# Kernel optimization log

Hardware: AMD Instinct MI355X
Metric: run time of the kernel (lower is better)

Reference implementation:

```python
import jax, jax.numpy as jnp
import numpy as np

KERNEL = 5
DILATIONS = (3, 1)
N_HEADS = 8
LN_EPS = 1e-5


def unfold1d(x, kernel, dilation, pad):
    # x: (N, H, S) -> (N, H, S, kernel) dilated sliding windows (same length)
    xp = jnp.pad(x, ((0, 0), (0, 0), (pad, pad)))
    S = x.shape[-1]
    idx = jnp.arange(S)[:, None] + jnp.arange(kernel)[None, :] * dilation  # (S, K)
    return xp[:, :, idx]  # (N, H, S, K)


def dilated_mha(q, k, v, Ws, bs, Wo, bo):
    # q,k,v: (B, S, D); Ws: (2, split, split); Wo: (D, D)
    B, S, D = q.shape
    ndil = len(DILATIONS)
    hpd = N_HEADS // ndil            # heads per dilation
    dk = D // N_HEADS
    split = D // ndil
    scale = dk ** (-0.5)
    outs, probs = [], []
    for i, dil in enumerate(DILATIONS):
        pad = dil * (KERNEL - 1) // 2
        sl = slice(i * split, (i + 1) * split)
        qi = q[..., sl] @ Ws[i].T + bs[i]
        ki = k[..., sl] @ Ws[i].T + bs[i]
        vi = v[..., sl] @ Ws[i].T + bs[i]
        # (B,S,hpd,dk) -> (B,dk,hpd,S), matching torch transpose(1,2).permute(0,3,1,2)
        to4 = lambda x: jnp.transpose(x.reshape(B, S, hpd, dk), (0, 3, 2, 1))
        qi4, ki4, vi4 = to4(qi), to4(ki), to4(vi)
        # unfold then reinterpret (B*dk,hpd,...) as (B*hpd,dk,...) exactly as torch .reshape does
        kp = unfold1d(ki4.reshape(B * dk, hpd, S), KERNEL, dil, pad).reshape(B * hpd, dk, S, KERNEL)
        vp = unfold1d(vi4.reshape(B * dk, hpd, S), KERNEL, dil, pad).reshape(B * hpd, dk, S, KERNEL)
        qr = qi4.reshape(B * hpd, dk, S)
        scores = jnp.einsum('nds,ndsk->nsk', qr, kp) * scale   # (B*hpd, S, K)
        p = jax.nn.softmax(scores, axis=-1)
        out = jnp.einsum('nsk,ndsk->nds', p, vp)               # (B*hpd, dk, S)
        out = jnp.transpose(out.reshape(B, hpd, dk, S), (0, 3, 1, 2)).reshape(B, S, split)
        outs.append(out)
        probs.append(p.reshape(B, hpd, S, KERNEL))
    o = jnp.concatenate(outs, axis=-1) @ Wo.T + bo
    return o, jnp.concatenate(probs, axis=1)


def layer_norm(x, g, b):
    mu = jnp.mean(x, axis=-1, keepdims=True)
    var = jnp.mean((x - mu) ** 2, axis=-1, keepdims=True)
    return (x - mu) * jax.lax.rsqrt(var + LN_EPS) * g + b


def setup_inputs() -> dict:
    key = jax.random.key(0)
    ks = jax.random.split(key, 6)
    B, S, D = 32, 2048, 256
    split = D // 2
    q_emb = jax.random.normal(ks[0], (B, S, D), dtype=jnp.float32)
    s_emb = jax.random.normal(ks[1], (B, S, D), dtype=jnp.float32)
    lens = jax.random.randint(ks[2], (B,), 5, S, dtype=jnp.int32)
    W_lin = jax.random.normal(ks[3], (3, 2, split, split), dtype=jnp.float32) * (split ** -0.5)
    b_lin = jnp.zeros((3, 2, split), dtype=jnp.float32)
    W_out = jax.random.normal(ks[4], (3, D, D), dtype=jnp.float32) * (D ** -0.5)
    b_out = jnp.zeros((3, D), dtype=jnp.float32)
    ln_g = jnp.ones((3, D), dtype=jnp.float32)
    ln_b = jnp.zeros((3, D), dtype=jnp.float32)
    return {"q_emb": q_emb, "s_emb": s_emb, "lens": lens, "W_lin": W_lin,
            "b_lin": b_lin, "W_out": W_out, "b_out": b_out, "ln_g": ln_g, "ln_b": ln_b}


def reference(q_emb, s_emb, lens, W_lin, b_lin, W_out, b_out, ln_g, ln_b):
    # CASTransformer.forward, shortcut=True path, eval mode (dropout=id, mask unused)
    a1, _ = dilated_mha(q_emb, q_emb, q_emb, W_lin[0], b_lin[0], W_out[0], b_out[0])
    hq = layer_norm(q_emb + a1, ln_g[0], ln_b[0])
    a2, q_scores = dilated_mha(s_emb, s_emb, s_emb, W_lin[1], b_lin[1], W_out[1], b_out[1])
    hs = layer_norm(s_emb + a2, ln_g[1], ln_b[1])
    a3, _ = dilated_mha(hq, hq, hs, W_lin[2], b_lin[2], W_out[2], b_out[2])
    z = layer_norm(hq + a3, ln_g[2], ln_b[2])
    return z, q_scores
```

## Files before the change

### kernel.cpp

```cpp
#include <hip/hip_runtime.h>
#include <hip/hip_bf16.h>

typedef __bf16 bf16x8 __attribute__((ext_vector_type(8)));
typedef float  f32x4  __attribute__((ext_vector_type(4)));
typedef unsigned int u32;
typedef u32 u32x4 __attribute__((ext_vector_type(4)));
typedef unsigned short ushort_t;

__device__ inline float bf2f(ushort_t h) {
    union { u32 u; float f; } v; v.u = ((u32)h) << 16; return v.f;
}
__device__ inline ushort_t f2bf(float f) {
    union { float f; u32 u; } v; v.f = f;
    u32 u = v.u;
    return (ushort_t)((u + 0x7fffu + ((u >> 16) & 1u)) >> 16);
}
__device__ inline bf16x8 load_bf8(const ushort_t* p) {
    u32x4 u = *reinterpret_cast<const u32x4*>(p);
    return __builtin_bit_cast(bf16x8, u);
}
__device__ inline bf16x8 load8_in(const void* base, size_t idx, int f32flag) {
    if (!f32flag) return load_bf8((const ushort_t*)base + idx);
    const float* pf = (const float*)base + idx;
    f32x4 a = *reinterpret_cast<const f32x4*>(pf);
    f32x4 b = *reinterpret_cast<const f32x4*>(pf + 4);
    bf16x8 r;
#pragma unroll
    for (int j = 0; j < 4; ++j) { r[j] = (__bf16)a[j]; r[4 + j] = (__bf16)b[j]; }
    return r;
}
__device__ inline float ld_in(const void* base, size_t idx, int f32flag) {
    return f32flag ? ((const float*)base)[idx] : bf2f(((const ushort_t*)base)[idx]);
}

#define XT_STRIDE 264

__global__ __launch_bounds__(256) void detect_kernel(const u32* __restrict__ d, int n,
                                                     int* __restrict__ flag) {
    const int t = threadIdx.x;
    int cn = 0, co = 0;
    for (int i = t; i < n; i += 256) {
        const u32 w = d[i];
        const u32 e  = (w >> 7) & 0xFF;
        const u32 fe = (w >> 23) & 0xFF;
        cn += (e >= 100 && e <= 135) ? 1 : 0;
        co += (((w & 0xFFFFu) == 0u) && fe >= 100 && fe <= 140) ? 1 : 0;
    }
    __shared__ int sn[256], so[256];
    sn[t] = cn; so[t] = co; __syncthreads();
    for (int o = 128; o; o >>= 1) {
        if (t < o) { sn[t] += sn[t + o]; so[t] += so[t + o]; }
        __syncthreads();
    }
    if (t == 0) {
        const int CN = sn[0], CO = so[0];
        const int is_f32 = (2 * CN < n) && ((2 * CO > n) || (20 * CN > n));
        *flag = is_f32 ? 1 : 0;
    }
}

__device__ inline int f_of(const int* flags, int i) { return i < 0 ? 0 : flags[i]; }
__device__ inline int out_f32(const int* flags) {
    return flags[0] | flags[1] | flags[3] | flags[4] | flags[5] | flags[6] | flags[7] | flags[8];
}

__global__ __launch_bounds__(256) void proj_kernel(
    const void* __restrict__ X, int xi,
    const void* __restrict__ W, size_t lw,
    const void* __restrict__ Bv, size_t lb,
    ushort_t* __restrict__ Y, const int* __restrict__ flags)
{
    const int xf = f_of(flags, xi);
    const int wf = flags[3], bf = flags[4];
    const int tid  = threadIdx.x;
    const int wave = tid >> 6, lane = tid & 63;
    const int dil  = wave >> 1;
    const int n_off = (wave & 1) * 64;
    const int m0   = blockIdx.x * 64;
    const int l15  = lane & 15, quad = lane >> 4;

    f32x4 acc[4][4] = {};
    for (int kc = 0; kc < 4; ++kc) {
        bf16x8 a[4], b[4];
#pragma unroll
        for (int mt = 0; mt < 4; ++mt)
            a[mt] = load8_in(X, (size_t)(m0 + mt * 16 + l15) * 256 + dil * 128 + kc * 32 + quad * 8, xf);
#pragma unroll
        for (int nt = 0; nt < 4; ++nt)
            b[nt] = load8_in(W, lw + (size_t)dil * 16384 + (size_t)(n_off + nt * 16 + l15) * 128 + kc * 32 + quad * 8, wf);
#pragma unroll
        for (int mt = 0; mt < 4; ++mt)
#pragma unroll
            for (int nt = 0; nt < 4; ++nt)
                acc[mt][nt] = __builtin_amdgcn_mfma_f32_16x16x32_bf16(a[mt], b[nt], acc[mt][nt], 0, 0, 0);
    }
#pragma unroll
    for (int mt = 0; mt < 4; ++mt) {
#pragma unroll
        for (int nt = 0; nt < 4; ++nt) {
            const int ncol = n_off + nt * 16 + l15;
            const float bias = ld_in(Bv, lb + dil * 128 + ncol, bf);
#pragma unroll
            for (int r = 0; r < 4; ++r) {
                const int row = m0 + mt * 16 + quad * 4 + r;
                Y[(size_t)row * 256 + dil * 128 + ncol] = f2bf(acc[mt][nt][r] + bias);
            }
        }
    }
}

__global__ __launch_bounds__(256) void proj_inplace_kernel(
    ushort_t* __restrict__ X,
    const void* __restrict__ W, size_t lw,
    const void* __restrict__ Bv, size_t lb,
    const int* __restrict__ flags)
{
    __shared__ ushort_t xt[64 * XT_STRIDE];
    const int wf = flags[3], bf = flags[4];
    const int tid = threadIdx.x;
    const int m0  = blockIdx.x * 64;
#pragma unroll
    for (int i = 0; i < 8; ++i) {
        const int chunk = tid + 256 * i;
        const int row = chunk >> 5, cc = chunk & 31;
        *reinterpret_cast<u32x4*>(&xt[row * XT_STRIDE + cc * 8]) =
            *reinterpret_cast<const u32x4*>(X + (size_t)(m0 + row) * 256 + cc * 8);
    }
    __syncthreads();

    const int wave = tid >> 6, lane = tid & 63;
    const int dil  = wave >> 1;
    const int n_off = (wave & 1) * 64;
    const int l15  = lane & 15, quad = lane >> 4;

    f32x4 acc[4][4] = {};
    for (int kc = 0; kc < 4; ++kc) {
        bf16x8 a[4], b[4];
#pragma unroll
        for (int mt = 0; mt < 4; ++mt)
            a[mt] = load_bf8(&xt[(mt * 16 + l15) * XT_STRIDE + dil * 128 + kc * 32 + quad * 8]);
#pragma unroll
        for (int nt = 0; nt < 4; ++nt)
            b[nt] = load8_in(W, lw + (size_t)dil * 16384 + (size_t)(n_off + nt * 16 + l15) * 128 + kc * 32 + quad * 8, wf);
#pragma unroll
        for (int mt = 0; mt < 4; ++mt)
#pragma unroll
            for (int nt = 0; nt < 4; ++nt)
                acc[mt][nt] = __builtin_amdgcn_mfma_f32_16x16x32_bf16(a[mt], b[nt], acc[mt][nt], 0, 0, 0);
    }
#pragma unroll
    for (int mt = 0; mt < 4; ++mt) {
#pragma unroll
        for (int nt = 0; nt < 4; ++nt) {
            const int ncol = n_off + nt * 16 + l15;
            const float bias = ld_in(Bv, lb + dil * 128 + ncol, bf);
#pragma unroll
            for (int r = 0; r < 4; ++r) {
                const int row = m0 + mt * 16 + quad * 4 + r;
                X[(size_t)row * 256 + dil * 128 + ncol] = f2bf(acc[mt][nt][r] + bias);
            }
        }
    }
}

__global__ __launch_bounds__(256) void fused_attn_oln_kernel(
    const ushort_t* __restrict__ P, const ushort_t* __restrict__ V,
    const void* __restrict__ R, int ri,
    const void* __restrict__ W, size_t lw,
    const void* __restrict__ Bv, size_t lb,
    const void* __restrict__ G, const void* __restrict__ Bt, size_t lg,
    void* __restrict__ H, int h_out,
    void* __restrict__ probs_base,
    const int* __restrict__ flags)
{
    __shared__ ushort_t xt[64 * XT_STRIDE];
    __shared__ float lsum[4][64], lsq[4][64];

    const int wf = flags[5], bvf = flags[6], gf = flags[7], btf = flags[8];
    const int rf = f_of(flags, ri);
    const int og = out_f32(flags);
    const int of = h_out ? og : 0;

    const int tid = threadIdx.x;
    const int m0  = blockIdx.x * 64;
    const int bb  = m0 >> 11;
    const int s0  = m0 & 2047;
    const size_t rowbase = (size_t)bb * 2048;
    const float scale = 0.17677669529663687f;

#pragma unroll
    for (int it = 0; it < 2; ++it) {
        const int task = tid + 256 * it;
        const int r  = task & 63;
        const int dg = task >> 6;
        const int dil = dg >> 2, g = dg & 3;
        const int dila = dil ? 1 : 3;
        const int s = s0 + r;
        const size_t chan0 = (size_t)dil * 128 + g * 8;

        const ushort_t* qr = P + (rowbase + s) * 256 + chan0;
        float qv[4][8];
#pragma unroll
        for (int h = 0; h < 4; ++h) {
            bf16x8 t = load_bf8(qr + h * 32);
#pragma unroll
            for (int j = 0; j < 8; ++j) qv[h][j] = (float)t[j];
        }
        float sc[5];
#pragma unroll
        for (int kk = 0; kk < 5; ++kk) {
            const int sp = s + (kk - 2) * dila;
            float a = 0.f;
            if (sp >= 0 && sp < 2048) {
                const ushort_t* kr = P + (rowbase + sp) * 256 + chan0;
#pragma unroll
                for (int h = 0; h < 4; ++h) {
                    bf16x8 t = load_bf8(kr + h * 32);
#pragma unroll
                    for (int j = 0; j < 8; ++j) a += qv[h][j] * (float)t[j];
                }
                a *= scale;
            }
            sc[kk] = a;
        }
        float mx = sc[0];
#pragma unroll
        for (int kk = 1; kk < 5; ++kk) mx = fmaxf(mx, sc[kk]);
        float p[5], sum = 0.f;
#pragma unroll
        for (int kk = 0; kk < 5; ++kk) { p[kk] = __expf(sc[kk] - mx); sum += p[kk]; }
        const float inv = 1.f / sum;
#pragma unroll
        for (int kk = 0; kk < 5; ++kk) p[kk] *= inv;

        float o[4][8] = {};
#pragma unroll
        for (int kk = 0; kk < 5; ++kk) {
            const int sp = s + (kk - 2) * dila;
            if (sp < 0 || sp >= 2048) continue;
            const ushort_t* vr = V + (rowbase + sp) * 256 + chan0;
#pragma unroll
            for (int h = 0; h < 4; ++h) {
                bf16x8 t = load_bf8(vr + h * 32);
#pragma unroll
                for (int j = 0; j < 8; ++j) o[h][j] += p[kk] * (float)t[j];
            }
        }
        ushort_t* op = &xt[r * XT_STRIDE + dil * 128 + g * 32];
#pragma unroll
        for (int c = 0; c < 4; ++c) {
            u32x4 w;
#pragma unroll
            for (int t4 = 0; t4 < 4; ++t4) {
                const int d2a = c * 8 + t4 * 2, d2b = d2a + 1;
                const u32 lo = f2bf(o[d2a & 3][d2a >> 2]);
                const u32 hi = f2bf(o[d2b & 3][d2b >> 2]);
                w[t4] = lo | (hi << 16);
            }
            *reinterpret_cast<u32x4*>(op + c * 8) = w;
        }
        if (probs_base != nullptr) {
            const size_t pb = 16777216 + ((size_t)((bb * 8 + dg) * 2048 + s)) * 5;
            if (og) {
                float* pp = (float*)probs_base;
#pragma unroll
                for (int kk = 0; kk < 5; ++kk) pp[pb + kk] = p[kk];
            } else {
                ushort_t* pp = (ushort_t*)probs_base;
#pragma unroll
                for (int kk = 0; kk < 5; ++kk) pp[pb + kk] = f2bf(p[kk]);
            }
        }
    }
    __syncthreads();

    const int wave = tid >> 6, lane = tid & 63;
    const int n_off = wave * 64;
    const int l15 = lane & 15, quad = lane >> 4;

    f32x4 acc[4][4] = {};
    for (int kc = 0; kc < 8; ++kc) {
        bf16x8 a[4], b[4];
#pragma unroll
        for (int mt = 0; mt < 4; ++mt)
            a[mt] = load_bf8(&xt[(mt * 16 + l15) * XT_STRIDE + kc * 32 + quad * 8]);
#pragma unroll
        for (int nt = 0; nt < 4; ++nt)
            b[nt] = load8_in(W, lw + (size_t)(n_off + nt * 16 + l15) * 256 + kc * 32 + quad * 8, wf);
#pragma unroll
        for (int mt = 0; mt < 4; ++mt)
#pragma unroll
            for (int nt = 0; nt < 4; ++nt)
                acc[mt][nt] = __builtin_amdgcn_mfma_f32_16x16x32_bf16(a[mt], b[nt], acc[mt][nt], 0, 0, 0);
    }

    float bias[4];
#pragma unroll
    for (int nt = 0; nt < 4; ++nt) bias[nt] = ld_in(Bv, lb + n_off + nt * 16 + l15, bvf);

    float psum[4][4] = {}, psq[4][4] = {};
#pragma unroll
    for (int mt = 0; mt < 4; ++mt) {
#pragma unroll
        for (int rr = 0; rr < 4; ++rr) {
            const size_t rrow = (size_t)(m0 + mt * 16 + quad * 4 + rr) * 256 + l15;
#pragma unroll
            for (int nt = 0; nt < 4; ++nt) {
                float v = acc[mt][nt][rr] + bias[nt] + ld_in(R, rrow + n_off + nt * 16, rf);
                acc[mt][nt][rr] = v;
                psum[mt][rr] += v;
                psq[mt][rr]  += v * v;
            }
        }
    }
#pragma unroll
    for (int off = 1; off <= 8; off <<= 1) {
#pragma unroll
        for (int mt = 0; mt < 4; ++mt)
#pragma unroll
            for (int rr = 0; rr < 4; ++rr) {
                psum[mt][rr] += __shfl_xor(psum[mt][rr], off);
                psq[mt][rr]  += __shfl_xor(psq[mt][rr],  off);
            }
    }
    if (l15 == 0) {
#pragma unroll
        for (int mt = 0; mt < 4; ++mt)
#pragma unroll
            for (int rr = 0; rr < 4; ++rr) {
                const int row = mt * 16 + quad * 4 + rr;
                lsum[wave][row] = psum[mt][rr];
                lsq[wave][row]  = psq[mt][rr];
            }
    }
    __syncthreads();

    float gl[4], bl[4];
#pragma unroll
    for (int nt = 0; nt < 4; ++nt) {
        gl[nt] = ld_in(G,  lg + n_off + nt * 16 + l15, gf);
        bl[nt] = ld_in(Bt, lg + n_off + nt * 16 + l15, btf);
    }
#pragma unroll
    for (int mt = 0; mt < 4; ++mt) {
#pragma unroll
        for (int rr = 0; rr < 4; ++rr) {
            const int row = mt * 16 + quad * 4 + rr;
            const float sm = lsum[0][row] + lsum[1][row] + lsum[2][row] + lsum[3][row];
            const float q2 = lsq[0][row]  + lsq[1][row]  + lsq[2][row]  + lsq[3][row];
            const float mu  = sm * (1.f / 256.f);
            const float var = q2 * (1.f / 256.f) - mu * mu;
            const float rs  = rsqrtf(var + 1e-5f);
            const size_t hrow = (size_t)(m0 + row) * 256 + l15;
#pragma unroll
            for (int nt = 0; nt < 4; ++nt) {
                const float hv = (acc[mt][nt][rr] - mu) * rs * gl[nt] + bl[nt];
                if (of) ((float*)H)[hrow + n_off + nt * 16] = hv;
                else    ((ushort_t*)H)[hrow + n_off + nt * 16] = f2bf(hv);
            }
        }
    }
}

extern "C" void kernel_launch(void* const* d_in, const int* in_sizes, int n_in,
                              void* d_out, int out_size, void* d_ws, size_t ws_size,
                              hipStream_t stream) {
    const void* q_emb = d_in[0];
    const void* s_emb = d_in[1];
    const void* W_lin = d_in[3];
    const void* b_lin = d_in[4];
    const void* W_out = d_in[5];
    const void* b_out = d_in[6];
    const void* ln_g  = d_in[7];
    const void* ln_b  = d_in[8];

    const size_t SLOT = 16777216;
    int*      flags = (int*)d_ws;
    ushort_t* SA = (ushort_t*)((char*)d_ws + 256);
    ushort_t* SB = SA + SLOT;
    ushort_t* SC = SA + 2 * SLOT;

    const dim3 blk(256);
    detect_kernel<<<1, blk, 0, stream>>>((const u32*)q_emb, 16384, flags + 0);
    detect_kernel<<<1, blk, 0, stream>>>((const u32*)s_emb, 16384, flags + 1);
    detect_kernel<<<1, blk, 0, stream>>>((const u32*)W_lin, 16384, flags + 3);
    detect_kernel<<<1, blk, 0, stream>>>((const u32*)b_lin,   384, flags + 4);
    detect_kernel<<<1, blk, 0, stream>>>((const u32*)W_out, 16384, flags + 5);
    detect_kernel<<<1, blk, 0, stream>>>((const u32*)b_out,   384, flags + 6);
    detect_kernel<<<1, blk, 0, stream>>>((const u32*)ln_g,    384, flags + 7);
    detect_kernel<<<1, blk, 0, stream>>>((const u32*)ln_b,    384, flags + 8);

    proj_kernel<<<1024, blk, 0, stream>>>(q_emb, 0, W_lin, 0, b_lin, 0, SC, flags);
    fused_attn_oln_kernel<<<1024, blk, 0, stream>>>(SC, SC, q_emb, 0,
        W_out, 0, b_out, 0, ln_g, ln_b, 0, SA, 0, nullptr, flags);
    proj_kernel<<<1024, blk, 0, stream>>>(s_emb, 1, W_lin, 32768, b_lin, 256, SC, flags);
    fused_attn_oln_kernel<<<1024, blk, 0, stream>>>(SC, SC, s_emb, 1,
        W_out, 65536, b_out, 256, ln_g, ln_b, 256, SB, 0, d_out, flags);
    proj_kernel<<<1024, blk, 0, stream>>>(SA, -1, W_lin, 65536, b_lin, 512, SC, flags);
    proj_inplace_kernel<<<1024, blk, 0, stream>>>(SB, W_lin, 65536, b_lin, 512, flags);
    fused_attn_oln_kernel<<<1024, blk, 0, stream>>>(SC, SB, SA, -1,
        W_out, 131072, b_out, 512, ln_g, ln_b, 512, d_out, 1, nullptr, flags);
}
```

Measured before the change: 696.1 us.

## Fuse input projection into attention+output stage kernel with halo tiles in LDS

Each stage now computes the per-dilation linear projection for a 64-row tile plus an 8-row halo on each side directly into a swizzled shared-memory tile, then runs the windowed attention from LDS instead of from a global projected buffer. This removes the separate projection kernels and the round trip of the projected activations through global memory, and it collapses seven launches into three. In exchange, each block recomputes 16 halo rows per tile (80 rows instead of 64), serializes the two dilations through more barriers, and uses a larger shared-memory footprint that may reduce occupancy.

After: 855.7 us. +22.9%, slower.

```diff
diff --git a/kernel.cpp b/kernel.cpp
--- a/kernel.cpp
+++ b/kernel.cpp
@@ -64,145 +64,95 @@
     return flags[0] | flags[1] | flags[3] | flags[4] | flags[5] | flags[6] | flags[7] | flags[8];
 }
 
-__global__ __launch_bounds__(256) void proj_kernel(
-    const void* __restrict__ X, int xi,
-    const void* __restrict__ W, size_t lw,
-    const void* __restrict__ Bv, size_t lb,
-    ushort_t* __restrict__ Y, const int* __restrict__ flags)
+__device__ inline int tidx(int row, int ch) { return row * 128 + (ch ^ ((row & 7) << 3)); }
+
+__device__ __forceinline__ void proj_tile(
+    const void* __restrict__ X, int xf, int dil, int bb, int s0,
+    const void* __restrict__ W, size_t lw, int wfl,
+    const void* __restrict__ Bv, size_t lb, int bfl,
+    ushort_t* tile, int wave, int lane)
 {
-    const int xf = f_of(flags, xi);
-    const int wf = flags[3], bf = flags[4];
-    const int tid  = threadIdx.x;
-    const int wave = tid >> 6, lane = tid & 63;
-    const int dil  = wave >> 1;
-    const int n_off = (wave & 1) * 64;
-    const int m0   = blockIdx.x * 64;
-    const int l15  = lane & 15, quad = lane >> 4;
-
-    f32x4 acc[4][4] = {};
+    const int l15 = lane & 15, quad = lane >> 4;
+    const int n_off = wave * 32;
+    f32x4 acc[5][2] = {};
     for (int kc = 0; kc < 4; ++kc) {
-        bf16x8 a[4], b[4];
-#pragma unroll
-        for (int mt = 0; mt < 4; ++mt)
-            a[mt] = load8_in(X, (size_t)(m0 + mt * 16 + l15) * 256 + dil * 128 + kc * 32 + quad * 8, xf);
-#pragma unroll
-        for (int nt = 0; nt < 4; ++nt)
-            b[nt] = load8_in(W, lw + (size_t)dil * 16384 + (size_t)(n_off + nt * 16 + l15) * 128 + kc * 32 + quad * 8, wf);
-#pragma unroll
-        for (int mt = 0; mt < 4; ++mt)
-#pragma unroll
-            for (int nt = 0; nt < 4; ++nt)
+        bf16x8 a[5], b[2];
+#pragma unroll
+        for (int mt = 0; mt < 5; ++mt) {
+            int s = s0 - 8 + mt * 16 + l15;
+            s = s < 0 ? 0 : (s > 2047 ? 2047 : s);
+            a[mt] = load8_in(X, ((size_t)bb * 2048 + s) * 256 + dil * 128 + kc * 32 + quad * 8, xf);
+        }
+#pragma unroll
+        for (int nt = 0; nt < 2; ++nt)
+            b[nt] = load8_in(W, lw + (size_t)dil * 16384 +
+                             (size_t)(n_off + nt * 16 + l15) * 128 + kc * 32 + quad * 8, wfl);
+#pragma unroll
+        for (int mt = 0; mt < 5; ++mt)
+#pragma unroll
+            for (int nt = 0; nt < 2; ++nt)
                 acc[mt][nt] = __builtin_amdgcn_mfma_f32_16x16x32_bf16(a[mt], b[nt], acc[mt][nt], 0, 0, 0);
     }
 #pragma unroll
-    for (int mt = 0; mt < 4; ++mt) {
-#pragma unroll
-        for (int nt = 0; nt < 4; ++nt) {
-            const int ncol = n_off + nt * 16 + l15;
-            const float bias = ld_in(Bv, lb + dil * 128 + ncol, bf);
+    for (int nt = 0; nt < 2; ++nt) {
+        const int ncol = n_off + nt * 16 + l15;
+        const float bias = ld_in(Bv, lb + dil * 128 + ncol, bfl);
+#pragma unroll
+        for (int mt = 0; mt < 5; ++mt)
 #pragma unroll
             for (int r = 0; r < 4; ++r) {
-                const int row = m0 + mt * 16 + quad * 4 + r;
-                Y[(size_t)row * 256 + dil * 128 + ncol] = f2bf(acc[mt][nt][r] + bias);
-            }
-        }
-    }
-}
-
-__global__ __launch_bounds__(256) void proj_inplace_kernel(
-    ushort_t* __restrict__ X,
-    const void* __restrict__ W, size_t lw,
-    const void* __restrict__ Bv, size_t lb,
-    const int* __restrict__ flags)
-{
-    __shared__ ushort_t xt[64 * XT_STRIDE];
-    const int wf = flags[3], bf = flags[4];
-    const int tid = threadIdx.x;
-    const int m0  = blockIdx.x * 64;
-#pragma unroll
-    for (int i = 0; i < 8; ++i) {
-        const int chunk = tid + 256 * i;
-        const int row = chunk >> 5, cc = chunk & 31;
-        *reinterpret_cast<u32x4*>(&xt[row * XT_STRIDE + cc * 8]) =
-            *reinterpret_cast<const u32x4*>(X + (size_t)(m0 + row) * 256 + cc * 8);
-    }
-    __syncthreads();
-
-    const int wave = tid >> 6, lane = tid & 63;
-    const int dil  = wave >> 1;
-    const int n_off = (wave & 1) * 64;
-    const int l15  = lane & 15, quad = lane >> 4;
-
-    f32x4 acc[4][4] = {};
-    for (int kc = 0; kc < 4; ++kc) {
-        bf16x8 a[4], b[4];
-#pragma unroll
-        for (int mt = 0; mt < 4; ++mt)
-            a[mt] = load_bf8(&xt[(mt * 16 + l15) * XT_STRIDE + dil * 128 + kc * 32 + quad * 8]);
-#pragma unroll
-        for (int nt = 0; nt < 4; ++nt)
-            b[nt] = load8_in(W, lw + (size_t)dil * 16384 + (size_t)(n_off + nt * 16 + l15) * 128 + kc * 32 + quad * 8, wf);
-#pragma unroll
-        for (int mt = 0; mt < 4; ++mt)
-#pragma unroll
-            for (int nt = 0; nt < 4; ++nt)
-                acc[mt][nt] = __builtin_amdgcn_mfma_f32_16x16x32_bf16(a[mt], b[nt], acc[mt][nt], 0, 0, 0);
-    }
-#pragma unroll
-    for (int mt = 0; mt < 4; ++mt) {
-#pragma unroll
-        for (int nt = 0; nt < 4; ++nt) {
-            const int ncol = n_off + nt * 16 + l15;
-            const float bias = ld_in(Bv, lb + dil * 128 + ncol, bf);
-#pragma unroll
-            for (int r = 0; r < 4; ++r) {
-                const int row = m0 + mt * 16 + quad * 4 + r;
-                X[(size_t)row * 256 + dil * 128 + ncol] = f2bf(acc[mt][nt][r] + bias);
-            }
-        }
-    }
-}
-
-__global__ __launch_bounds__(256) void fused_attn_oln_kernel(
-    const ushort_t* __restrict__ P, const ushort_t* __restrict__ V,
+                const int row = mt * 16 + quad * 4 + r;
+                tile[tidx(row, ncol)] = f2bf(acc[mt][nt][r] + bias);
+            }
+    }
+}
+
+__global__ __launch_bounds__(256) void stage_kernel(
+    const void* __restrict__ Xq, int xqi,
+    const void* __restrict__ Xv, int xvi, int sepv,
+    const void* __restrict__ Wl, size_t lwl,
+    const void* __restrict__ bl, size_t lbl,
+    const void* __restrict__ Wo, size_t lwo,
+    const void* __restrict__ bo, size_t lbo,
+    const void* __restrict__ G, const void* __restrict__ Bt, size_t lg,
     const void* __restrict__ R, int ri,
-    const void* __restrict__ W, size_t lw,
-    const void* __restrict__ Bv, size_t lb,
-    const void* __restrict__ G, const void* __restrict__ Bt, size_t lg,
     void* __restrict__ H, int h_out,
     void* __restrict__ probs_base,
     const int* __restrict__ flags)
 {
-    __shared__ ushort_t xt[64 * XT_STRIDE];
-    __shared__ float lsum[4][64], lsq[4][64];
-
-    const int wf = flags[5], bvf = flags[6], gf = flags[7], btf = flags[8];
-    const int rf = f_of(flags, ri);
-    const int og = out_f32(flags);
-    const int of = h_out ? og : 0;
-
-    const int tid = threadIdx.x;
-    const int m0  = blockIdx.x * 64;
-    const int bb  = m0 >> 11;
-    const int s0  = m0 & 2047;
-    const size_t rowbase = (size_t)bb * 2048;
+    __shared__ __align__(16) char smem[54272];
+    ushort_t* tile = (ushort_t*)smem;
+    ushort_t* xt   = (ushort_t*)(smem + 20480);
+
+    const int xqf = f_of(flags, xqi), xvf = f_of(flags, xvi);
+    const int wlf = flags[3], blf = flags[4];
+    const int wof = flags[5], bof = flags[6], gf = flags[7], btf = flags[8];
+    const int rf  = f_of(flags, ri);
+    const int og  = out_f32(flags);
+    const int of  = h_out ? og : 0;
+
+    const int tid  = threadIdx.x;
+    const int wave = tid >> 6, lane = tid & 63;
+    const int l15  = lane & 15, quad = lane >> 4;
+    const int m0   = blockIdx.x * 64;
+    const int bb   = m0 >> 11;
+    const int s0   = m0 & 2047;
     const float scale = 0.17677669529663687f;
 
-#pragma unroll
-    for (int it = 0; it < 2; ++it) {
-        const int task = tid + 256 * it;
-        const int r  = task & 63;
-        const int dg = task >> 6;
-        const int dil = dg >> 2, g = dg & 3;
+    const int r = lane, g = wave;
+
+    for (int dil = 0; dil < 2; ++dil) {
+        if (dil) __syncthreads();
+        proj_tile(Xq, xqf, dil, bb, s0, Wl, lwl, wlf, bl, lbl, blf, tile, wave, lane);
+        __syncthreads();
+
         const int dila = dil ? 1 : 3;
         const int s = s0 + r;
-        const size_t chan0 = (size_t)dil * 128 + g * 8;
-
-        const ushort_t* qr = P + (rowbase + s) * 256 + chan0;
+
         float qv[4][8];
 #pragma unroll
         for (int h = 0; h < 4; ++h) {
-            bf16x8 t = load_bf8(qr + h * 32);
+            bf16x8 t = load_bf8(&tile[tidx(8 + r, g * 8 + h * 32)]);
 #pragma unroll
             for (int j = 0; j < 8; ++j) qv[h][j] = (float)t[j];
         }
@@ -212,10 +162,10 @@
             const int sp = s + (kk - 2) * dila;
             float a = 0.f;
             if (sp >= 0 && sp < 2048) {
-                const ushort_t* kr = P + (rowbase + sp) * 256 + chan0;
+                const int krow = 8 + r + (kk - 2) * dila;
 #pragma unroll
                 for (int h = 0; h < 4; ++h) {
-                    bf16x8 t = load_bf8(kr + h * 32);
+                    bf16x8 t = load_bf8(&tile[tidx(krow, g * 8 + h * 32)]);
 #pragma unroll
                     for (int j = 0; j < 8; ++j) a += qv[h][j] * (float)t[j];
                 }
@@ -233,15 +183,34 @@
 #pragma unroll
         for (int kk = 0; kk < 5; ++kk) p[kk] *= inv;
 
+        if (probs_base != nullptr) {
+            const size_t pb = 16777216 + ((size_t)((bb * 8 + dil * 4 + g) * 2048 + s)) * 5;
+            if (og) {
+                float* pp = (float*)probs_base;
+#pragma unroll
+                for (int kk = 0; kk < 5; ++kk) pp[pb + kk] = p[kk];
+            } else {
+                ushort_t* pp = (ushort_t*)probs_base;
+#pragma unroll
+                for (int kk = 0; kk < 5; ++kk) pp[pb + kk] = f2bf(p[kk]);
+            }
+        }
+
+        if (sepv) {
+            __syncthreads();
+            proj_tile(Xv, xvf, dil, bb, s0, Wl, lwl, wlf, bl, lbl, blf, tile, wave, lane);
+            __syncthreads();
+        }
+
         float o[4][8] = {};
 #pragma unroll
         for (int kk = 0; kk < 5; ++kk) {
             const int sp = s + (kk - 2) * dila;
             if (sp < 0 || sp >= 2048) continue;
-            const ushort_t* vr = V + (rowbase + sp) * 256 + chan0;
+            const int vrow = 8 + r + (kk - 2) * dila;
 #pragma unroll
             for (int h = 0; h < 4; ++h) {
-                bf16x8 t = load_bf8(vr + h * 32);
+                bf16x8 t = load_bf8(&tile[tidx(vrow, g * 8 + h * 32)]);
 #pragma unroll
                 for (int j = 0; j < 8; ++j) o[h][j] += p[kk] * (float)t[j];
             }
@@ -259,24 +228,13 @@
             }
             *reinterpret_cast<u32x4*>(op + c * 8) = w;
         }
-        if (probs_base != nullptr) {
-            const size_t pb = 16777216 + ((size_t)((bb * 8 + dg) * 2048 + s)) * 5;
-            if (og) {
-                float* pp = (float*)probs_base;
-#pragma unroll
-                for (int kk = 0; kk < 5; ++kk) pp[pb + kk] = p[kk];
-            } else {
-                ushort_t* pp = (ushort_t*)probs_base;
-#pragma unroll
-                for (int kk = 0; kk < 5; ++kk) pp[pb + kk] = f2bf(p[kk]);
-            }
-        }
     }
     __syncthreads();
 
-    const int wave = tid >> 6, lane = tid & 63;
+    float (*lsum)[64] = (float(*)[64])(smem);
+    float (*lsq)[64]  = (float(*)[64])(smem + 1024);
+
     const int n_off = wave * 64;
-    const int l15 = lane & 15, quad = lane >> 4;
 
     f32x4 acc[4][4] = {};
     for (int kc = 0; kc < 8; ++kc) {
@@ -286,7 +244,7 @@
             a[mt] = load_bf8(&xt[(mt * 16 + l15) * XT_STRIDE + kc * 32 + quad * 8]);
 #pragma unroll
         for (int nt = 0; nt < 4; ++nt)
-            b[nt] = load8_in(W, lw + (size_t)(n_off + nt * 16 + l15) * 256 + kc * 32 + quad * 8, wf);
+            b[nt] = load8_in(Wo, lwo + (size_t)(n_off + nt * 16 + l15) * 256 + kc * 32 + quad * 8, wof);
 #pragma unroll
         for (int mt = 0; mt < 4; ++mt)
 #pragma unroll
@@ -296,7 +254,7 @@
 
     float bias[4];
 #pragma unroll
-    for (int nt = 0; nt < 4; ++nt) bias[nt] = ld_in(Bv, lb + n_off + nt * 16 + l15, bvf);
+    for (int nt = 0; nt < 4; ++nt) bias[nt] = ld_in(bo, lbo + n_off + nt * 16 + l15, bof);
 
     float psum[4][4] = {}, psq[4][4] = {};
 #pragma unroll
@@ -335,11 +293,11 @@
     }
     __syncthreads();
 
-    float gl[4], bl[4];
+    float gl[4], blv[4];
 #pragma unroll
     for (int nt = 0; nt < 4; ++nt) {
-        gl[nt] = ld_in(G,  lg + n_off + nt * 16 + l15, gf);
-        bl[nt] = ld_in(Bt, lg + n_off + nt * 16 + l15, btf);
+        gl[nt]  = ld_in(G,  lg + n_off + nt * 16 + l15, gf);
+        blv[nt] = ld_in(Bt, lg + n_off + nt * 16 + l15, btf);
     }
 #pragma unroll
     for (int mt = 0; mt < 4; ++mt) {
@@ -354,7 +312,7 @@
             const size_t hrow = (size_t)(m0 + row) * 256 + l15;
 #pragma unroll
             for (int nt = 0; nt < 4; ++nt) {
-                const float hv = (acc[mt][nt][rr] - mu) * rs * gl[nt] + bl[nt];
+                const float hv = (acc[mt][nt][rr] - mu) * rs * gl[nt] + blv[nt];
                 if (of) ((float*)H)[hrow + n_off + nt * 16] = hv;
                 else    ((ushort_t*)H)[hrow + n_off + nt * 16] = f2bf(hv);
             }
@@ -378,7 +336,6 @@
     int*      flags = (int*)d_ws;
     ushort_t* SA = (ushort_t*)((char*)d_ws + 256);
     ushort_t* SB = SA + SLOT;
-    ushort_t* SC = SA + 2 * SLOT;
 
     const dim3 blk(256);
     detect_kernel<<<1, blk, 0, stream>>>((const u32*)q_emb, 16384, flags + 0);
@@ -390,14 +347,13 @@
     detect_kernel<<<1, blk, 0, stream>>>((const u32*)ln_g,    384, flags + 7);
     detect_kernel<<<1, blk, 0, stream>>>((const u32*)ln_b,    384, flags + 8);
 
-    proj_kernel<<<1024, blk, 0, stream>>>(q_emb, 0, W_lin, 0, b_lin, 0, SC, flags);
-    fused_attn_oln_kernel<<<1024, blk, 0, stream>>>(SC, SC, q_emb, 0,
-        W_out, 0, b_out, 0, ln_g, ln_b, 0, SA, 0, nullptr, flags);
-    proj_kernel<<<1024, blk, 0, stream>>>(s_emb, 1, W_lin, 32768, b_lin, 256, SC, flags);
-    fused_attn_oln_kernel<<<1024, blk, 0, stream>>>(SC, SC, s_emb, 1,
-        W_out, 65536, b_out, 256, ln_g, ln_b, 256, SB, 0, d_out, flags);
-    proj_kernel<<<1024, blk, 0, stream>>>(SA, -1, W_lin, 65536, b_lin, 512, SC, flags);
-    proj_inplace_kernel<<<1024, blk, 0, stream>>>(SB, W_lin, 65536, b_lin, 512, flags);
-    fused_attn_oln_kernel<<<1024, blk, 0, stream>>>(SC, SB, SA, -1,
-        W_out, 131072, b_out, 512, ln_g, ln_b, 512, d_out, 1, nullptr, flags);
-}
+    stage_kernel<<<1024, blk, 0, stream>>>(q_emb, 0, q_emb, 0, 0,
+        W_lin, 0, b_lin, 0, W_out, 0, b_out, 0, ln_g, ln_b, 0,
+        q_emb, 0, SA, 0, nullptr, flags);
+    stage_kernel<<<1024, blk, 0, stream>>>(s_emb, 1, s_emb, 1, 0,
+        W_lin, 32768, b_lin, 256, W_out, 65536, b_out, 256, ln_g, ln_b, 256,
+        s_emb, 1, SB, 0, d_out, flags);
+    stage_kernel<<<1024, blk, 0, stream>>>(SA, -1, SB, -1, 1,
+        W_lin, 65536, b_lin, 512, W_out, 131072, b_out, 512, ln_g, ln_b, 512,
+        SA, -1, d_out, 1, nullptr, flags);
+}
```

## Stage Q/K/V halo tiles in swizzled LDS and coalesce projection stores

Applied to the files above, without the earlier changes.

The attention kernel now loads a 64-row tile plus an 8-row halo of the projected Q/K (and V when it differs) into shared memory with an XOR swizzle. The dilated window reads then come from LDS instead of strided global loads. The projection kernel stages its input tile in swizzled LDS and writes results back through LDS so global stores are coalesced 16-byte vectors. The separate in-place projection kernel is merged into it. Launch bounds now request 4 blocks per SM. This adds more LDS per block (40 KB in attention) and extra barriers, which may limit occupancy.

After: 621.8 us. -10.7%, faster.

```diff
diff --git a/kernel.cpp b/kernel.cpp
--- a/kernel.cpp
+++ b/kernel.cpp
@@ -33,7 +33,8 @@
     return f32flag ? ((const float*)base)[idx] : bf2f(((const ushort_t*)base)[idx]);
 }
 
-#define XT_STRIDE 264
+__device__ inline int pofs(int row, int ch) { return row * 256 + (ch ^ ((row & 15) << 3)); }
+__device__ inline int tofs(int tr, int ch) { return tr * 256 + (ch ^ (((tr + 8) & 15) << 3)); }
 
 __global__ __launch_bounds__(256) void detect_kernel(const u32* __restrict__ d, int n,
                                                      int* __restrict__ flag) {
@@ -64,67 +65,24 @@
     return flags[0] | flags[1] | flags[3] | flags[4] | flags[5] | flags[6] | flags[7] | flags[8];
 }
 
-__global__ __launch_bounds__(256) void proj_kernel(
+__global__ __launch_bounds__(256, 4) void proj_kernel(
     const void* __restrict__ X, int xi,
     const void* __restrict__ W, size_t lw,
     const void* __restrict__ Bv, size_t lb,
     ushort_t* __restrict__ Y, const int* __restrict__ flags)
 {
-    const int xf = f_of(flags, xi);
-    const int wf = flags[3], bf = flags[4];
-    const int tid  = threadIdx.x;
-    const int wave = tid >> 6, lane = tid & 63;
-    const int dil  = wave >> 1;
-    const int n_off = (wave & 1) * 64;
-    const int m0   = blockIdx.x * 64;
-    const int l15  = lane & 15, quad = lane >> 4;
-
-    f32x4 acc[4][4] = {};
-    for (int kc = 0; kc < 4; ++kc) {
-        bf16x8 a[4], b[4];
-#pragma unroll
-        for (int mt = 0; mt < 4; ++mt)
-            a[mt] = load8_in(X, (size_t)(m0 + mt * 16 + l15) * 256 + dil * 128 + kc * 32 + quad * 8, xf);
-#pragma unroll
-        for (int nt = 0; nt < 4; ++nt)
-            b[nt] = load8_in(W, lw + (size_t)dil * 16384 + (size_t)(n_off + nt * 16 + l15) * 128 + kc * 32 + quad * 8, wf);
-#pragma unroll
-        for (int mt = 0; mt < 4; ++mt)
-#pragma unroll
-            for (int nt = 0; nt < 4; ++nt)
-                acc[mt][nt] = __builtin_amdgcn_mfma_f32_16x16x32_bf16(a[mt], b[nt], acc[mt][nt], 0, 0, 0);
-    }
-#pragma unroll
-    for (int mt = 0; mt < 4; ++mt) {
-#pragma unroll
-        for (int nt = 0; nt < 4; ++nt) {
-            const int ncol = n_off + nt * 16 + l15;
-            const float bias = ld_in(Bv, lb + dil * 128 + ncol, bf);
-#pragma unroll
-            for (int r = 0; r < 4; ++r) {
-                const int row = m0 + mt * 16 + quad * 4 + r;
-                Y[(size_t)row * 256 + dil * 128 + ncol] = f2bf(acc[mt][nt][r] + bias);
-            }
-        }
-    }
-}
-
-__global__ __launch_bounds__(256) void proj_inplace_kernel(
-    ushort_t* __restrict__ X,
-    const void* __restrict__ W, size_t lw,
-    const void* __restrict__ Bv, size_t lb,
-    const int* __restrict__ flags)
-{
-    __shared__ ushort_t xt[64 * XT_STRIDE];
-    const int wf = flags[3], bf = flags[4];
+    __shared__ ushort_t tile[64 * 256];
+    const int xf  = f_of(flags, xi);
+    const int wf  = flags[3], bfl = flags[4];
     const int tid = threadIdx.x;
     const int m0  = blockIdx.x * 64;
+
 #pragma unroll
     for (int i = 0; i < 8; ++i) {
-        const int chunk = tid + 256 * i;
-        const int row = chunk >> 5, cc = chunk & 31;
-        *reinterpret_cast<u32x4*>(&xt[row * XT_STRIDE + cc * 8]) =
-            *reinterpret_cast<const u32x4*>(X + (size_t)(m0 + row) * 256 + cc * 8);
+        const int c = tid + 256 * i;
+        const int row = c >> 5, cc = c & 31;
+        bf16x8 v = load8_in(X, (size_t)(m0 + row) * 256 + cc * 8, xf);
+        *reinterpret_cast<u32x4*>(&tile[pofs(row, cc * 8)]) = __builtin_bit_cast(u32x4, v);
     }
     __syncthreads();
 
@@ -138,32 +96,43 @@
         bf16x8 a[4], b[4];
 #pragma unroll
         for (int mt = 0; mt < 4; ++mt)
-            a[mt] = load_bf8(&xt[(mt * 16 + l15) * XT_STRIDE + dil * 128 + kc * 32 + quad * 8]);
+            a[mt] = load_bf8(&tile[pofs(mt * 16 + l15, dil * 128 + kc * 32 + quad * 8)]);
 #pragma unroll
         for (int nt = 0; nt < 4; ++nt)
-            b[nt] = load8_in(W, lw + (size_t)dil * 16384 + (size_t)(n_off + nt * 16 + l15) * 128 + kc * 32 + quad * 8, wf);
+            b[nt] = load8_in(W, lw + (size_t)dil * 16384 +
+                             (size_t)(n_off + nt * 16 + l15) * 128 + kc * 32 + quad * 8, wf);
 #pragma unroll
         for (int mt = 0; mt < 4; ++mt)
 #pragma unroll
             for (int nt = 0; nt < 4; ++nt)
                 acc[mt][nt] = __builtin_amdgcn_mfma_f32_16x16x32_bf16(a[mt], b[nt], acc[mt][nt], 0, 0, 0);
     }
-#pragma unroll
-    for (int mt = 0; mt < 4; ++mt) {
-#pragma unroll
-        for (int nt = 0; nt < 4; ++nt) {
-            const int ncol = n_off + nt * 16 + l15;
-            const float bias = ld_in(Bv, lb + dil * 128 + ncol, bf);
+    __syncthreads();
+
+#pragma unroll
+    for (int nt = 0; nt < 4; ++nt) {
+        const int ncol = n_off + nt * 16 + l15;
+        const float bias = ld_in(Bv, lb + dil * 128 + ncol, bfl);
+#pragma unroll
+        for (int mt = 0; mt < 4; ++mt)
 #pragma unroll
             for (int r = 0; r < 4; ++r) {
-                const int row = m0 + mt * 16 + quad * 4 + r;
-                X[(size_t)row * 256 + dil * 128 + ncol] = f2bf(acc[mt][nt][r] + bias);
-            }
-        }
-    }
-}
-
-__global__ __launch_bounds__(256) void fused_attn_oln_kernel(
+                const int row = mt * 16 + quad * 4 + r;
+                tile[pofs(row, dil * 128 + ncol)] = f2bf(acc[mt][nt][r] + bias);
+            }
+    }
+    __syncthreads();
+
+#pragma unroll
+    for (int i = 0; i < 8; ++i) {
+        const int c = tid + 256 * i;
+        const int row = c >> 5, cc = c & 31;
+        *reinterpret_cast<u32x4*>(Y + (size_t)(m0 + row) * 256 + cc * 8) =
+            *reinterpret_cast<const u32x4*>(&tile[row * 256 + cc * 8]);
+    }
+}
+
+__global__ __launch_bounds__(256, 4) void fused_attn_oln_kernel(
     const ushort_t* __restrict__ P, const ushort_t* __restrict__ V,
     const void* __restrict__ R, int ri,
     const void* __restrict__ W, size_t lw,
@@ -173,36 +142,48 @@
     void* __restrict__ probs_base,
     const int* __restrict__ flags)
 {
-    __shared__ ushort_t xt[64 * XT_STRIDE];
-    __shared__ float lsum[4][64], lsq[4][64];
+    __shared__ ushort_t tile[80 * 256];
+    float (*lsum)[64] = (float (*)[64])(&tile[0]);
+    float (*lsq)[64]  = (float (*)[64])(&tile[1024]);
 
     const int wf = flags[5], bvf = flags[6], gf = flags[7], btf = flags[8];
     const int rf = f_of(flags, ri);
     const int og = out_f32(flags);
     const int of = h_out ? og : 0;
 
-    const int tid = threadIdx.x;
-    const int m0  = blockIdx.x * 64;
-    const int bb  = m0 >> 11;
-    const int s0  = m0 & 2047;
+    const int tid  = threadIdx.x;
+    const int wave = tid >> 6, lane = tid & 63;
+    const int l15  = lane & 15, quad = lane >> 4;
+    const int m0   = blockIdx.x * 64;
+    const int bb   = m0 >> 11;
+    const int s0   = m0 & 2047;
     const size_t rowbase = (size_t)bb * 2048;
     const float scale = 0.17677669529663687f;
 
 #pragma unroll
+    for (int i = 0; i < 10; ++i) {
+        const int c = tid + 256 * i;
+        const int tr = c >> 5, cc = c & 31;
+        int s = s0 - 8 + tr; s = s < 0 ? 0 : (s > 2047 ? 2047 : s);
+        *reinterpret_cast<u32x4*>(&tile[tr * 256 + cc * 8]) =
+            *reinterpret_cast<const u32x4*>(P + (rowbase + s) * 256 + cc * 8);
+    }
+    __syncthreads();
+
+    const int r = lane, g = wave;
+    const int s = s0 + r;
+
+    float p2[2][5];
+#pragma unroll
     for (int it = 0; it < 2; ++it) {
-        const int task = tid + 256 * it;
-        const int r  = task & 63;
-        const int dg = task >> 6;
-        const int dil = dg >> 2, g = dg & 3;
+        const int dil  = it;
         const int dila = dil ? 1 : 3;
-        const int s = s0 + r;
-        const size_t chan0 = (size_t)dil * 128 + g * 8;
-
-        const ushort_t* qr = P + (rowbase + s) * 256 + chan0;
+        const int ch0  = dil * 128 + g * 8;
+
         float qv[4][8];
 #pragma unroll
         for (int h = 0; h < 4; ++h) {
-            bf16x8 t = load_bf8(qr + h * 32);
+            bf16x8 t = load_bf8(&tile[tofs(8 + r, ch0 + h * 32)]);
 #pragma unroll
             for (int j = 0; j < 8; ++j) qv[h][j] = (float)t[j];
         }
@@ -212,10 +193,10 @@
             const int sp = s + (kk - 2) * dila;
             float a = 0.f;
             if (sp >= 0 && sp < 2048) {
-                const ushort_t* kr = P + (rowbase + sp) * 256 + chan0;
+                const int tr2 = 8 + r + (kk - 2) * dila;
 #pragma unroll
                 for (int h = 0; h < 4; ++h) {
-                    bf16x8 t = load_bf8(kr + h * 32);
+                    bf16x8 t = load_bf8(&tile[tofs(tr2, ch0 + h * 32)]);
 #pragma unroll
                     for (int j = 0; j < 8; ++j) a += qv[h][j] * (float)t[j];
                 }
@@ -226,27 +207,59 @@
         float mx = sc[0];
 #pragma unroll
         for (int kk = 1; kk < 5; ++kk) mx = fmaxf(mx, sc[kk]);
-        float p[5], sum = 0.f;
-#pragma unroll
-        for (int kk = 0; kk < 5; ++kk) { p[kk] = __expf(sc[kk] - mx); sum += p[kk]; }
+        float sum = 0.f;
+#pragma unroll
+        for (int kk = 0; kk < 5; ++kk) { p2[it][kk] = __expf(sc[kk] - mx); sum += p2[it][kk]; }
         const float inv = 1.f / sum;
 #pragma unroll
-        for (int kk = 0; kk < 5; ++kk) p[kk] *= inv;
-
+        for (int kk = 0; kk < 5; ++kk) p2[it][kk] *= inv;
+
+        if (probs_base != nullptr) {
+            const size_t pb = 16777216 + ((size_t)((bb * 8 + dil * 4 + g) * 2048 + s)) * 5;
+            if (og) {
+                float* pp = (float*)probs_base;
+#pragma unroll
+                for (int kk = 0; kk < 5; ++kk) pp[pb + kk] = p2[it][kk];
+            } else {
+                ushort_t* pp = (ushort_t*)probs_base;
+#pragma unroll
+                for (int kk = 0; kk < 5; ++kk) pp[pb + kk] = f2bf(p2[it][kk]);
+            }
+        }
+    }
+
+    if (V != P) {
+        __syncthreads();
+#pragma unroll
+        for (int i = 0; i < 10; ++i) {
+            const int c = tid + 256 * i;
+            const int tr = c >> 5, cc = c & 31;
+            int s2 = s0 - 8 + tr; s2 = s2 < 0 ? 0 : (s2 > 2047 ? 2047 : s2);
+            *reinterpret_cast<u32x4*>(&tile[tr * 256 + cc * 8]) =
+                *reinterpret_cast<const u32x4*>(V + (rowbase + s2) * 256 + cc * 8);
+        }
+        __syncthreads();
+    }
+
+    u32x4 wpk[2][4];
+#pragma unroll
+    for (int it = 0; it < 2; ++it) {
+        const int dil  = it;
+        const int dila = dil ? 1 : 3;
+        const int ch0  = dil * 128 + g * 8;
         float o[4][8] = {};
 #pragma unroll
         for (int kk = 0; kk < 5; ++kk) {
             const int sp = s + (kk - 2) * dila;
             if (sp < 0 || sp >= 2048) continue;
-            const ushort_t* vr = V + (rowbase + sp) * 256 + chan0;
+            const int tr2 = 8 + r + (kk - 2) * dila;
 #pragma unroll
             for (int h = 0; h < 4; ++h) {
-                bf16x8 t = load_bf8(vr + h * 32);
-#pragma unroll
-                for (int j = 0; j < 8; ++j) o[h][j] += p[kk] * (float)t[j];
-            }
-        }
-        ushort_t* op = &xt[r * XT_STRIDE + dil * 128 + g * 32];
+                bf16x8 t = load_bf8(&tile[tofs(tr2, ch0 + h * 32)]);
+#pragma unroll
+                for (int j = 0; j < 8; ++j) o[h][j] += p2[it][kk] * (float)t[j];
+            }
+        }
 #pragma unroll
         for (int c = 0; c < 4; ++c) {
             u32x4 w;
@@ -257,33 +270,26 @@
                 const u32 hi = f2bf(o[d2b & 3][d2b >> 2]);
                 w[t4] = lo | (hi << 16);
             }
-            *reinterpret_cast<u32x4*>(op + c * 8) = w;
-        }
-        if (probs_base != nullptr) {
-            const size_t pb = 16777216 + ((size_t)((bb * 8 + dg) * 2048 + s)) * 5;
-            if (og) {
-                float* pp = (float*)probs_base;
-#pragma unroll
-                for (int kk = 0; kk < 5; ++kk) pp[pb + kk] = p[kk];
-            } else {
-                ushort_t* pp = (ushort_t*)probs_base;
-#pragma unroll
-                for (int kk = 0; kk < 5; ++kk) pp[pb + kk] = f2bf(p[kk]);
-            }
-        }
-    }
-    __syncthreads();
-
-    const int wave = tid >> 6, lane = tid & 63;
+            wpk[it][c] = w;
+        }
+    }
+    __syncthreads();
+
+#pragma unroll
+    for (int it = 0; it < 2; ++it)
+#pragma unroll
+        for (int c = 0; c < 4; ++c)
+            *reinterpret_cast<u32x4*>(&tile[tofs(8 + r, it * 128 + g * 32 + c * 8)]) = wpk[it][c];
+    __syncthreads();
+
     const int n_off = wave * 64;
-    const int l15 = lane & 15, quad = lane >> 4;
 
     f32x4 acc[4][4] = {};
     for (int kc = 0; kc < 8; ++kc) {
         bf16x8 a[4], b[4];
 #pragma unroll
         for (int mt = 0; mt < 4; ++mt)
-            a[mt] = load_bf8(&xt[(mt * 16 + l15) * XT_STRIDE + kc * 32 + quad * 8]);
+            a[mt] = load_bf8(&tile[tofs(8 + mt * 16 + l15, kc * 32 + quad * 8)]);
 #pragma unroll
         for (int nt = 0; nt < 4; ++nt)
             b[nt] = load8_in(W, lw + (size_t)(n_off + nt * 16 + l15) * 256 + kc * 32 + quad * 8, wf);
@@ -335,11 +341,11 @@
     }
     __syncthreads();
 
-    float gl[4], bl[4];
+    float gl[4], blv[4];
 #pragma unroll
     for (int nt = 0; nt < 4; ++nt) {
-        gl[nt] = ld_in(G,  lg + n_off + nt * 16 + l15, gf);
-        bl[nt] = ld_in(Bt, lg + n_off + nt * 16 + l15, btf);
+        gl[nt]  = ld_in(G,  lg + n_off + nt * 16 + l15, gf);
+        blv[nt] = ld_in(Bt, lg + n_off + nt * 16 + l15, btf);
     }
 #pragma unroll
     for (int mt = 0; mt < 4; ++mt) {
@@ -354,7 +360,7 @@
             const size_t hrow = (size_t)(m0 + row) * 256 + l15;
 #pragma unroll
             for (int nt = 0; nt < 4; ++nt) {
-                const float hv = (acc[mt][nt][rr] - mu) * rs * gl[nt] + bl[nt];
+                const float hv = (acc[mt][nt][rr] - mu) * rs * gl[nt] + blv[nt];
                 if (of) ((float*)H)[hrow + n_off + nt * 16] = hv;
                 else    ((ushort_t*)H)[hrow + n_off + nt * 16] = f2bf(hv);
             }
@@ -397,7 +403,7 @@
     fused_attn_oln_kernel<<<1024, blk, 0, stream>>>(SC, SC, s_emb, 1,
         W_out, 65536, b_out, 256, ln_g, ln_b, 256, SB, 0, d_out, flags);
     proj_kernel<<<1024, blk, 0, stream>>>(SA, -1, W_lin, 65536, b_lin, 512, SC, flags);
-    proj_inplace_kernel<<<1024, blk, 0, stream>>>(SB, W_lin, 65536, b_lin, 512, flags);
+    proj_kernel<<<1024, blk, 0, stream>>>(SB, -1, W_lin, 65536, b_lin, 512, SB, flags);
     fused_attn_oln_kernel<<<1024, blk, 0, stream>>>(SC, SB, SA, -1,
         W_out, 131072, b_out, 512, ln_g, ln_b, 512, d_out, 1, nullptr, flags);
 }
```
